# Kernel tuning notes

Measured on AMD Instinct MI355X. Metric: run time of the kernel, lower is better.

The kernel has to match this reference:

```python
import jax, jax.numpy as jnp
import numpy as np

EARLY_ROUND = 6
LATE_ROUND = 12
NUM_CLASSES = 35


def setup_inputs() -> dict:
    key = jax.random.key(0)
    k1, k2, k3 = jax.random.split(key, 3)
    B = 1048576
    logits = jax.random.normal(k1, (B, NUM_CLASSES), dtype=jnp.float32)
    targets = jax.random.randint(k2, (B,), 0, NUM_CLASSES, dtype=jnp.int64)
    turns = jax.random.randint(k3, (B,), 0, 24, dtype=jnp.int64)
    return {"logits": logits, "targets": targets, "turns": turns}


def reference(logits, targets, turns):
    # per-sample cross entropy (reduction='none')
    logp = jax.nn.log_softmax(logits, axis=-1)  # [B, C]
    losses = -jnp.take_along_axis(logp, targets[:, None], axis=-1)[:, 0]  # [B]
    # piecewise-linear weight: 0.7 for turn<=early, 1.0 for turn>=late, lerp between
    t = turns.astype(logits.dtype)
    frac = (t - EARLY_ROUND) / (LATE_ROUND - EARLY_ROUND)
    weights = jnp.clip(0.7 + 0.3 * frac, 0.7, 1.0)
    return jnp.mean(losses * weights)
```

## Files before the change

kernel.cpp:

```cpp
#include <hip/hip_runtime.h>
#include <math.h>

#define NUM_CLASSES 35
#define ROWS_PER_BLOCK 256

__global__ __launch_bounds__(256) void fuzzy_loss_pass1(
    const float* __restrict__ logits,
    const int* __restrict__ targets,
    const int* __restrict__ turns,
    float* __restrict__ block_sums)
{
    __shared__ float lds[ROWS_PER_BLOCK * NUM_CLASSES];
    const int tid  = threadIdx.x;
    const int row0 = blockIdx.x * ROWS_PER_BLOCK;
    const int row  = row0 + tid;

    const int tgt = targets[row];
    const int trn = turns[row];

    {
        const float* src = logits + (size_t)row0 * NUM_CLASSES;
        #pragma unroll
        for (int i = 0; i < 8; ++i) {
            const int idx = tid + i * ROWS_PER_BLOCK;
            __builtin_amdgcn_global_load_lds(
                (const __attribute__((address_space(1))) void*)(src + (size_t)idx * 4),
                (__attribute__((address_space(3))) void*)(lds + (size_t)idx * 4),
                16, 0, 0);
        }
        if (tid < 192) {
            const int idx = 8 * ROWS_PER_BLOCK + tid;
            __builtin_amdgcn_global_load_lds(
                (const __attribute__((address_space(1))) void*)(src + (size_t)idx * 4),
                (__attribute__((address_space(3))) void*)(lds + (size_t)idx * 4),
                16, 0, 0);
        }
    }
    __syncthreads();

    const float* r = lds + tid * NUM_CLASSES;

    float s = 0.0f;
    #pragma unroll
    for (int j = 0; j < NUM_CLASSES; ++j) s += __expf(r[j]);

    const float xt = r[tgt];
    float loss = __logf(s) - xt;

    float w = fmaf(0.05f, (float)trn, 0.4f);
    w = fminf(fmaxf(w, 0.7f), 1.0f);
    float v = loss * w;

    #pragma unroll
    for (int off = 32; off > 0; off >>= 1)
        v += __shfl_down(v, off, 64);

    __shared__ float wsum[ROWS_PER_BLOCK / 64];
    if ((tid & 63) == 0) wsum[tid >> 6] = v;
    __syncthreads();
    if (tid == 0)
        block_sums[blockIdx.x] = wsum[0] + wsum[1] + wsum[2] + wsum[3];
}

__global__ __launch_bounds__(256) void fuzzy_loss_pass2(
    const float* __restrict__ block_sums,
    float* __restrict__ out,
    int nblocks, float inv_B)
{
    const int tid = threadIdx.x;
    float v = 0.0f;
    const float4* src = (const float4*)block_sums;
    for (int i = tid; i < nblocks / 4; i += 256) {
        float4 f = src[i];
        v += (f.x + f.y) + (f.z + f.w);
    }
    #pragma unroll
    for (int off = 32; off > 0; off >>= 1)
        v += __shfl_down(v, off, 64);

    __shared__ float wsum[4];
    if ((tid & 63) == 0) wsum[tid >> 6] = v;
    __syncthreads();
    if (tid == 0)
        out[0] = (wsum[0] + wsum[1] + wsum[2] + wsum[3]) * inv_B;
}

extern "C" void kernel_launch(void* const* d_in, const int* in_sizes, int n_in,
                              void* d_out, int out_size, void* d_ws, size_t ws_size,
                              hipStream_t stream) {
    const float* logits  = (const float*)d_in[0];
    const int*   targets = (const int*)d_in[1];
    const int*   turns   = (const int*)d_in[2];
    float*       out     = (float*)d_out;
    float*       partial = (float*)d_ws;

    const int B = in_sizes[1];
    const int blocks = B / ROWS_PER_BLOCK;

    fuzzy_loss_pass1<<<blocks, ROWS_PER_BLOCK, 0, stream>>>(logits, targets, turns, partial);
    fuzzy_loss_pass2<<<1, 256, 0, stream>>>(partial, out, blocks, 1.0f / (float)B);
}
```

Measured before the change: 211.3 us.

## Use persistent blocks with double-buffered LDS tile prefetch

Replaces the one-tile-per-block launch with 512 persistent blocks. Each block walks 8 tiles and uses two LDS buffers, issuing the async global-to-LDS loads for the next tile while it computes the current one, with manual vmcnt waits and barriers. This aims to hide memory latency and cut launch and tail overhead, at the cost of doubling LDS per block, which lowers occupancy. It also relies on hand-tuned waitcnt values that must match the number of loads issued per tile.

```diff
diff --git a/kernel.cpp b/kernel.cpp
--- a/kernel.cpp
+++ b/kernel.cpp
@@ -2,61 +2,92 @@
 #include <math.h>
 
 #define NUM_CLASSES 35
-#define ROWS_PER_BLOCK 256
+#define ROWS_PER_TILE 256
+#define THREADS 256
+#define GRID_BLOCKS 512
+#define TILE_FLOATS (ROWS_PER_TILE * NUM_CLASSES)
+#define FULL16 8
+#define REM_OFF_B (FULL16 * THREADS * 16)
+
+__device__ __forceinline__ void stage_tile(const float* __restrict__ src,
+                                           float* __restrict__ dstlds, int tid)
+{
+    #pragma unroll
+    for (int i = 0; i < FULL16; ++i) {
+        const int byteoff = (tid + i * THREADS) * 16;
+        __builtin_amdgcn_global_load_lds(
+            (const __attribute__((address_space(1))) void*)((const char*)src + byteoff),
+            (__attribute__((address_space(3))) void*)((char*)dstlds + byteoff),
+            16, 0, 0);
+    }
+    {
+        const int byteoff = REM_OFF_B + tid * 12;
+        __builtin_amdgcn_global_load_lds(
+            (const __attribute__((address_space(1))) void*)((const char*)src + byteoff),
+            (__attribute__((address_space(3))) void*)((char*)dstlds + byteoff),
+            12, 0, 0);
+    }
+}
 
 __global__ __launch_bounds__(256) void fuzzy_loss_pass1(
     const float* __restrict__ logits,
     const int* __restrict__ targets,
     const int* __restrict__ turns,
-    float* __restrict__ block_sums)
+    float* __restrict__ block_sums,
+    int tiles_per_block)
 {
-    __shared__ float lds[ROWS_PER_BLOCK * NUM_CLASSES];
-    const int tid  = threadIdx.x;
-    const int row0 = blockIdx.x * ROWS_PER_BLOCK;
-    const int row  = row0 + tid;
+    __shared__ float buf0[TILE_FLOATS];
+    __shared__ float buf1[TILE_FLOATS];
+    __shared__ float wsum[THREADS / 64];
 
-    const int tgt = targets[row];
-    const int trn = turns[row];
+    const int tid   = threadIdx.x;
+    const int tile0 = blockIdx.x * tiles_per_block;
 
-    {
-        const float* src = logits + (size_t)row0 * NUM_CLASSES;
+    int tgt = targets[tile0 * ROWS_PER_TILE + tid];
+    int trn = turns[tile0 * ROWS_PER_TILE + tid];
+    stage_tile(logits + (size_t)tile0 * TILE_FLOATS, buf0, tid);
+    asm volatile("" ::: "memory");
+
+    float vacc = 0.0f;
+
+    for (int k = 0; k < tiles_per_block; ++k) {
+        float* cur = (k & 1) ? buf1 : buf0;
+        float* nxt = (k & 1) ? buf0 : buf1;
+
+        int ntgt = 0, ntrn = 0;
+        if (k < tiles_per_block - 1) {
+            const int nrow = (tile0 + k + 1) * ROWS_PER_TILE + tid;
+            ntgt = targets[nrow];
+            ntrn = turns[nrow];
+            stage_tile(logits + (size_t)(tile0 + k + 1) * TILE_FLOATS, nxt, tid);
+            asm volatile("s_waitcnt vmcnt(11)" ::: "memory");
+        } else {
+            asm volatile("s_waitcnt vmcnt(0)" ::: "memory");
+        }
+        __builtin_amdgcn_s_barrier();
+        asm volatile("" ::: "memory");
+
+        const float* r = cur + tid * NUM_CLASSES;
+        float s = 0.0f;
         #pragma unroll
-        for (int i = 0; i < 8; ++i) {
-            const int idx = tid + i * ROWS_PER_BLOCK;
-            __builtin_amdgcn_global_load_lds(
-                (const __attribute__((address_space(1))) void*)(src + (size_t)idx * 4),
-                (__attribute__((address_space(3))) void*)(lds + (size_t)idx * 4),
-                16, 0, 0);
-        }
-        if (tid < 192) {
-            const int idx = 8 * ROWS_PER_BLOCK + tid;
-            __builtin_amdgcn_global_load_lds(
-                (const __attribute__((address_space(1))) void*)(src + (size_t)idx * 4),
-                (__attribute__((address_space(3))) void*)(lds + (size_t)idx * 4),
-                16, 0, 0);
+        for (int j = 0; j < NUM_CLASSES; ++j) s += __expf(r[j]);
+        const float loss = __logf(s) - r[tgt];
+        float w = fmaf(0.05f, (float)trn, 0.4f);
+        w = fminf(fmaxf(w, 0.7f), 1.0f);
+        vacc = fmaf(loss, w, vacc);
+
+        if (k < tiles_per_block - 1) {
+            asm volatile("s_waitcnt lgkmcnt(0)" ::: "memory");
+            __builtin_amdgcn_s_barrier();
+            asm volatile("" ::: "memory");
+            tgt = ntgt; trn = ntrn;
         }
     }
-    __syncthreads();
-
-    const float* r = lds + tid * NUM_CLASSES;
-
-    float s = 0.0f;
-    #pragma unroll
-    for (int j = 0; j < NUM_CLASSES; ++j) s += __expf(r[j]);
-
-    const float xt = r[tgt];
-    float loss = __logf(s) - xt;
-
-    float w = fmaf(0.05f, (float)trn, 0.4f);
-    w = fminf(fmaxf(w, 0.7f), 1.0f);
-    float v = loss * w;
 
     #pragma unroll
     for (int off = 32; off > 0; off >>= 1)
-        v += __shfl_down(v, off, 64);
-
-    __shared__ float wsum[ROWS_PER_BLOCK / 64];
-    if ((tid & 63) == 0) wsum[tid >> 6] = v;
+        vacc += __shfl_down(vacc, off, 64);
+    if ((tid & 63) == 0) wsum[tid >> 6] = vacc;
     __syncthreads();
     if (tid == 0)
         block_sums[blockIdx.x] = wsum[0] + wsum[1] + wsum[2] + wsum[3];
@@ -95,8 +126,10 @@
     float*       partial = (float*)d_ws;
 
     const int B = in_sizes[1];
-    const int blocks = B / ROWS_PER_BLOCK;
+    const int total_tiles = B / ROWS_PER_TILE;
+    const int tpb = total_tiles / GRID_BLOCKS;
 
-    fuzzy_loss_pass1<<<blocks, ROWS_PER_BLOCK, 0, stream>>>(logits, targets, turns, partial);
-    fuzzy_loss_pass2<<<1, 256, 0, stream>>>(partial, out, blocks, 1.0f / (float)B);
+    fuzzy_loss_pass1<<<GRID_BLOCKS, THREADS, 0, stream>>>(
+        logits, targets, turns, partial, tpb);
+    fuzzy_loss_pass2<<<1, 256, 0, stream>>>(partial, out, GRID_BLOCKS, 1.0f / (float)B);
 }
```

Measured after the change: 215.2 us. No clear change (+1.8%).
